# Kernel optimization log

Hardware: AMD Instinct MI355X
Metric: run time of the kernel (lower is better)

Reference implementation:

```python
import jax, jax.numpy as jnp
import numpy as np

N = 50000   # nodes
E = 800000  # edges
C = 64      # node feature channels (0e)
A = 4       # edge attr channels
B = 16      # edge embedding (radial basis) size
H = 8       # radial MLP hidden size
D = 32      # query/key channels
P = 16      # node attr channels
R_MAX = 5.0


def setup_inputs() -> dict:
    key = jax.random.key(0)
    ks = jax.random.split(key, 20)
    w = lambda k, shape, fan_in: (jax.random.normal(k, shape, jnp.float32) / np.sqrt(fan_in).astype(np.float32))
    inp = {
        "node_feats": jax.random.normal(ks[0], (N, C), jnp.float32),
        "node_attrs": jax.random.normal(ks[1], (N, P), jnp.float32),
        "edge_embedding": jax.random.uniform(ks[2], (E, B), jnp.float32),
        "edge_attrs": jax.random.normal(ks[3], (E, A), jnp.float32),
        "positions": jax.random.normal(ks[4], (N, 3), jnp.float32) * 0.3,  # keep lengths < r_max
        "edge_src": jax.random.randint(ks[5], (E,), 0, N),
        "edge_dst": jax.random.randint(ks[6], (E,), 0, N),
        # parameters
        "W_q": w(ks[7], (C, D), C),            # h_q Linear
        "W1_k": w(ks[8], (B, H), B),           # radial MLP for tp_k
        "W2_k": w(ks[9], (H, C * A), H),
        "W1_v": w(ks[10], (B, H), B),          # radial MLP for tp_v
        "W2_v": w(ks[11], (H, C * A), H),
        "W_lin_k": w(ks[12], (C, D), C),       # linear_k
        "W_lin_v": w(ks[13], (C, C), C),       # linear_v
        "W_dot": w(ks[14], (D, D), D * D),     # FullyConnectedTensorProduct(q,k,'0e')
        "W_sc": w(ks[15], (C, P, C), C * P),   # self connection FCTP
    }
    return inp


def soft_unit_step(x):
    safe = jnp.where(x > 0, x, 1.0)
    return jnp.where(x > 0, jnp.exp(-1.0 / safe), 0.0)


def uvu_tp(x_src, edge_attrs, edge_embedding, W1, W2):
    # radial MLP -> per-edge, per-path weights [E, C, A]; 'uvu' tensor product on scalars
    wgt = (jax.nn.silu(edge_embedding @ W1) @ W2).reshape(-1, C, A)
    return x_src * (jnp.einsum('eca,ea->ec', wgt, edge_attrs) / np.sqrt(A).astype(np.float32))


def reference(node_feats, node_attrs, edge_embedding, edge_attrs, positions,
              edge_src, edge_dst, W_q, W1_k, W2_k, W1_v, W2_v,
              W_lin_k, W_lin_v, W_dot, W_sc):
    q = (node_feats @ W_q)[edge_dst]                              # [E, D]
    x_src = node_feats[edge_src]                                  # [E, C]
    k = uvu_tp(x_src, edge_attrs, edge_embedding, W1_k, W2_k) @ W_lin_k  # [E, D]
    v = uvu_tp(x_src, edge_attrs, edge_embedding, W1_v, W2_v) @ W_lin_v  # [E, C]

    edge_vec = positions[edge_dst] - positions[edge_src]
    edge_length = jnp.linalg.norm(edge_vec, axis=1)               # [E]
    cutoff = soft_unit_step(2.0 * R_MAX * (1.0 - edge_length / R_MAX))

    score = jnp.einsum('ei,ij,ej->e', q, W_dot, k)                # weighted bilinear dot -> 0e
    expv = cutoff * jnp.exp(score)                                # [E]
    z = jax.ops.segment_sum(expv, edge_dst, num_segments=N)       # softmax normalizer
    z = jnp.where(z == 0, 1.0, z)
    alpha = expv / z[edge_dst]
    msg = jnp.sqrt(jax.nn.relu(alpha))[:, None] * v               # [E, C]
    node_out = jax.ops.segment_sum(msg, edge_dst, num_segments=N)  # [N, C]

    sc = jnp.einsum('nc,np,cpo->no', node_feats, node_attrs, W_sc)
    return node_out + sc
```

## Files before the change

### kernel.cpp

```cpp
#include <hip/hip_runtime.h>
#include <math.h>

#define NN 50000
#define EE 800000
#define NPAD 50176

typedef __attribute__((ext_vector_type(8))) short short8v;
typedef __attribute__((ext_vector_type(4))) float f32x4;

static __device__ __forceinline__ short bf16r(float x) {
  union { float f; unsigned u; } v; v.f = x;
  unsigned r = v.u + 0x7FFFu + ((v.u >> 16) & 1u);
  return (short)(r >> 16);
}
static __device__ __forceinline__ float bf2f(unsigned u) {
  union { unsigned u; float f; } v; v.u = u << 16;
  return v.f;
}
static __device__ __forceinline__ unsigned pk2(float a, float b) {
  return (unsigned)(unsigned short)bf16r(a) | ((unsigned)(unsigned short)bf16r(b) << 16);
}


__global__ __launch_bounds__(256) void prep_kernel(
    const float* __restrict__ Wq, const float* __restrict__ Wdot,
    const float* __restrict__ Wlk, const float* __restrict__ W2k,
    const float* __restrict__ W2v, const float* __restrict__ Wlv,
    const float* __restrict__ Wsc, float* __restrict__ M,
    unsigned short* __restrict__ w2kT, unsigned short* __restrict__ w2vT,
    unsigned short* __restrict__ wlvb, unsigned short* __restrict__ wscb,
    int* __restrict__ cur)
{
  const int tid = threadIdx.x;
  const int b = blockIdx.x;
  if (b == 0) {
    __shared__ float tmp[2048];
#pragma unroll
    for (int r = 0; r < 8; ++r) {
      int idx = tid + r * 256;
      int cin = idx >> 5, d = idx & 31;
      float a = 0.f;
      for (int j = 0; j < 32; ++j) a = fmaf(Wq[cin * 32 + j], Wdot[j * 32 + d], a);
      tmp[idx] = a;
    }
    __syncthreads();
#pragma unroll
    for (int r = 0; r < 16; ++r) {
      int idx = tid + r * 256;
      int cin = idx >> 6, c = idx & 63;
      float a = 0.f;
      for (int d = 0; d < 32; ++d) a = fmaf(tmp[cin * 32 + d], Wlk[c * 32 + d], a);
      M[idx] = a;
    }
#pragma unroll
    for (int r = 0; r < 8; ++r) {
      int idx = tid + r * 256;
      int c = idx >> 5, k = idx & 31, h = k >> 2, a = k & 3;
      w2kT[idx] = (unsigned short)bf16r(W2k[h * 256 + c * 4 + a]);
      w2vT[idx] = (unsigned short)bf16r(W2v[h * 256 + c * 4 + a]);
    }
#pragma unroll
    for (int r = 0; r < 16; ++r) {
      int idx = tid + r * 256;
      int o = idx >> 6, c = idx & 63;
      wlvb[idx] = (unsigned short)bf16r(Wlv[c * 64 + o]);
    }
  } else if (b <= 196) {
    cur[(b - 1) * 256 + tid] = 0;
  } else {
    int w = (b - 197) * 256 + tid;
    int c = w & 63, o = (w >> 6) & 63, p = w >> 12;
    wscb[w] = (unsigned short)bf16r(Wsc[c * 1024 + p * 64 + o]);
  }
}

__global__ __launch_bounds__(256) void hist_zero(
    const int* __restrict__ edst, int* __restrict__ cur, float4* __restrict__ zu)
{
  int i = blockIdx.x * 256 + threadIdx.x;
  float4 zf = make_float4(0.f, 0.f, 0.f, 0.f);
  zu[i] = zf;
  if (i < 12544) zu[800000 + i] = zf;
  atomicAdd(&cur[edst[i]], 1);
}

__global__ __launch_bounds__(256) void scanA_kernel(
    int* __restrict__ cur, int* __restrict__ bsum)
{
  __shared__ int s[256];
  const int tid = threadIdx.x;
  const int i = blockIdx.x * 256 + tid;
  int v = cur[i];
  s[tid] = v;
  __syncthreads();
  for (int off = 1; off < 256; off <<= 1) {
    int t = (tid >= off) ? s[tid - off] : 0;
    __syncthreads();
    s[tid] += t;
    __syncthreads();
  }
  cur[i] = s[tid] - v;
  if (tid == 255) bsum[blockIdx.x] = s[255];
}

__global__ __launch_bounds__(256) void scanB_kernel(int* __restrict__ bsum)
{
  __shared__ int s[256];
  const int tid = threadIdx.x;
  int v = (tid < 196) ? bsum[tid] : 0;
  s[tid] = v;
  __syncthreads();
  for (int off = 1; off < 256; off <<= 1) {
    int t = (tid >= off) ? s[tid - off] : 0;
    __syncthreads();
    s[tid] += t;
    __syncthreads();
  }
  if (tid < 196) bsum[tid] = s[tid] - v;
}

__global__ __launch_bounds__(256) void scatter_fused(
    const int* __restrict__ esrc, const int* __restrict__ edst,
    const float* __restrict__ ea, const float* __restrict__ eb,
    const float* __restrict__ pos, const float* __restrict__ W1k,
    const float* __restrict__ W1v, int* __restrict__ cur,
    const int* __restrict__ bsum, int* __restrict__ perm,
    float* __restrict__ rec)
{
  int e = blockIdx.x * 256 + threadIdx.x;
  int s = esrc[e], d = edst[e];
  int r = atomicAdd(&cur[d], 1) + bsum[d >> 8];
  perm[r] = e;
  float dx = pos[d * 3 + 0] - pos[s * 3 + 0];
  float dy = pos[d * 3 + 1] - pos[s * 3 + 1];
  float dz = pos[d * 3 + 2] - pos[s * 3 + 2];
  float len = sqrtf(fmaf(dx, dx, fmaf(dy, dy, dz * dz)));
  float arg = 10.f - 2.f * len;
  float cl = (arg > 0.f) ? __expf(-1.f / arg) : 0.f;
  const f32x4* eb4 = reinterpret_cast<const f32x4*>(eb);
  f32x4 q0 = eb4[e * 4 + 0], q1 = eb4[e * 4 + 1],
        q2 = eb4[e * 4 + 2], q3 = eb4[e * 4 + 3];
  float ebv[16] = {q0.x, q0.y, q0.z, q0.w, q1.x, q1.y, q1.z, q1.w,
                   q2.x, q2.y, q2.z, q2.w, q3.x, q3.y, q3.z, q3.w};
  float h[16];
#pragma unroll
  for (int j = 0; j < 16; ++j) h[j] = 0.f;
#pragma unroll
  for (int b = 0; b < 16; ++b) {
    float x = ebv[b];
#pragma unroll
    for (int j = 0; j < 8; ++j) {
      h[j]     = fmaf(x, W1k[b * 8 + j], h[j]);
      h[8 + j] = fmaf(x, W1v[b * 8 + j], h[8 + j]);
    }
  }
#pragma unroll
  for (int j = 0; j < 16; ++j) h[j] = h[j] / (1.f + __expf(-h[j]));

  f32x4 a4 = reinterpret_cast<const f32x4*>(ea)[e];
  f32x4* rp4 = reinterpret_cast<f32x4*>(rec + (size_t)e * 12);
  f32x4 w0, w1, w2;
  w0.x = cl;
  w0.y = __uint_as_float(pk2(a4.x, a4.y));
  w0.z = __uint_as_float(pk2(a4.z, a4.w));
  w0.w = 0.f;
  w1.x = __uint_as_float(pk2(h[0], h[1]));
  w1.y = __uint_as_float(pk2(h[2], h[3]));
  w1.z = __uint_as_float(pk2(h[4], h[5]));
  w1.w = __uint_as_float(pk2(h[6], h[7]));
  w2.x = __uint_as_float(pk2(h[8], h[9]));
  w2.y = __uint_as_float(pk2(h[10], h[11]));
  w2.z = __uint_as_float(pk2(h[12], h[13]));
  w2.w = __uint_as_float(pk2(h[14], h[15]));
  rp4[0] = w0;
  rp4[1] = w1;
  rp4[2] = w2;
}

__global__ __launch_bounds__(256) void tq_kernel(
    const float* __restrict__ nf, const float* __restrict__ M, float* __restrict__ tq)
{
  __shared__ float Ml[4096];
  __shared__ float nfl[64 * 68];
  const int tid = threadIdx.x;
  const int base = blockIdx.x * 64;
#pragma unroll
  for (int r = 0; r < 4; ++r) {
    int idx = tid + r * 256;
    reinterpret_cast<float4*>(Ml)[idx] = reinterpret_cast<const float4*>(M)[idx];
  }
#pragma unroll
  for (int r = 0; r < 4; ++r) {
    int idx = tid + r * 256;
    int row = idx >> 4, c4 = idx & 15;
    float4 v = make_float4(0.f, 0.f, 0.f, 0.f);
    if (base + row < NN) v = reinterpret_cast<const float4*>(nf)[(base + row) * 16 + c4];
    *reinterpret_cast<float4*>(&nfl[row * 68 + c4 * 4]) = v;
  }
  __syncthreads();
  const int to = tid & 15, tn = tid >> 4;
  float4 acc[4] = {make_float4(0,0,0,0), make_float4(0,0,0,0),
                   make_float4(0,0,0,0), make_float4(0,0,0,0)};
  for (int c = 0; c < 64; ++c) {
    float4 m = reinterpret_cast<const float4*>(Ml)[c * 16 + to];
#pragma unroll
    for (int i = 0; i < 4; ++i) {
      float x = nfl[(tn * 4 + i) * 68 + c];
      acc[i].x = fmaf(x, m.x, acc[i].x);
      acc[i].y = fmaf(x, m.y, acc[i].y);
      acc[i].z = fmaf(x, m.z, acc[i].z);
      acc[i].w = fmaf(x, m.w, acc[i].w);
    }
  }
#pragma unroll
  for (int i = 0; i < 4; ++i) {
    int n = base + tn * 4 + i;
    if (n < NN) reinterpret_cast<float4*>(tq)[n * 16 + to] = acc[i];
  }
}

__global__ __launch_bounds__(256) void edge_kernel(
    const float* __restrict__ nf, const float* __restrict__ tq,
    const float* __restrict__ rec, const int* __restrict__ perm,
    const int* __restrict__ esrc, const int* __restrict__ edst,
    const unsigned short* __restrict__ w2kT, const unsigned short* __restrict__ w2vT,
    float* __restrict__ z, float* __restrict__ U)
{
  __shared__ float xsAll[4][16 * 68];
  __shared__ int   esAll[4][16];
  __shared__ int   edAll[4][16];
  __shared__ float clAll[4][16];
  __shared__ float evAll[4][16];
  const int tid  = threadIdx.x;
  const int lane = tid & 63;
  const int w = tid >> 6;
  const int lo = lane & 15, hi = lane >> 4;
  const int sb = (blockIdx.x * 4 + w) * 16;
  float* xs = xsAll[w];
  int*   es = esAll[w];
  int*   ed = edAll[w];
  float* cl = clAll[w];
  float* evs = evAll[w];

  short8v bk[4], bv[4];
#pragma unroll
  for (int t = 0; t < 4; ++t) {
    bk[t] = *reinterpret_cast<const short8v*>(&w2kT[(16 * t + lo) * 32 + hi * 8]);
    bv[t] = *reinterpret_cast<const short8v*>(&w2vT[(16 * t + lo) * 32 + hi * 8]);
  }

  const int eL = perm[sb + lo];
  const unsigned* ru = reinterpret_cast<const unsigned*>(rec);
  const size_t rb = (size_t)eL * 12;
  unsigned ea01 = ru[rb + 1];
  unsigned ea23 = ru[rb + 2];
  unsigned k01  = ru[rb + 4 + hi];
  unsigned v01  = ru[rb + 8 + hi];

  if (hi == 0) {
    es[lo] = esrc[eL];
    ed[lo] = edst[eL];
    cl[lo] = rec[rb];
  }
  __builtin_amdgcn_wave_barrier();

#pragma unroll
  for (int r = 0; r < 4; ++r) {
    int idx = lane + r * 64;
    int e = idx >> 4, c4 = idx & 15;
    float4 xv = reinterpret_cast<const float4*>(nf)[es[e] * 16 + c4];
    *reinterpret_cast<float4*>(&xs[e * 68 + c4 * 4]) = xv;
  }

  float ax = bf2f(ea01 & 0xffffu), ay = bf2f(ea01 >> 16);
  float az = bf2f(ea23 & 0xffffu), aw = bf2f(ea23 >> 16);
  float hk0 = bf2f(k01 & 0xffffu), hk1 = bf2f(k01 >> 16);
  float hv0 = bf2f(v01 & 0xffffu), hv1 = bf2f(v01 >> 16);
  short8v ak, av;
  ak[0] = bf16r(hk0 * ax); ak[1] = bf16r(hk0 * ay);
  ak[2] = bf16r(hk0 * az); ak[3] = bf16r(hk0 * aw);
  ak[4] = bf16r(hk1 * ax); ak[5] = bf16r(hk1 * ay);
  ak[6] = bf16r(hk1 * az); ak[7] = bf16r(hk1 * aw);
  av[0] = bf16r(hv0 * ax); av[1] = bf16r(hv0 * ay);
  av[2] = bf16r(hv0 * az); av[3] = bf16r(hv0 * aw);
  av[4] = bf16r(hv1 * ax); av[5] = bf16r(hv1 * ay);
  av[6] = bf16r(hv1 * az); av[7] = bf16r(hv1 * aw);
  __builtin_amdgcn_wave_barrier();

  f32x4 zero = {0.f, 0.f, 0.f, 0.f};
  f32x4 ack[4], acv[4];
#pragma unroll
  for (int t = 0; t < 4; ++t) {
    ack[t] = __builtin_amdgcn_mfma_f32_16x16x32_bf16(ak, bk[t], zero, 0, 0, 0);
    acv[t] = __builtin_amdgcn_mfma_f32_16x16x32_bf16(av, bv[t], zero, 0, 0, 0);
  }

  const int erow = 4 * hi;
  float p0, p1, p2, p3;
  {
    const float* x0 = &xs[(erow + 0) * 68 + lo];
    const float* x1 = &xs[(erow + 1) * 68 + lo];
    const float* x2 = &xs[(erow + 2) * 68 + lo];
    const float* x3 = &xs[(erow + 3) * 68 + lo];
    const float* t0 = tq + (size_t)ed[erow + 0] * 64 + lo;
    const float* t1 = tq + (size_t)ed[erow + 1] * 64 + lo;
    const float* t2 = tq + (size_t)ed[erow + 2] * 64 + lo;
    const float* t3 = tq + (size_t)ed[erow + 3] * 64 + lo;
    p0 = (x0[0]*t0[0])*ack[0][0] + (x0[16]*t0[16])*ack[1][0] + (x0[32]*t0[32])*ack[2][0] + (x0[48]*t0[48])*ack[3][0];
    p1 = (x1[0]*t1[0])*ack[0][1] + (x1[16]*t1[16])*ack[1][1] + (x1[32]*t1[32])*ack[2][1] + (x1[48]*t1[48])*ack[3][1];
    p2 = (x2[0]*t2[0])*ack[0][2] + (x2[16]*t2[16])*ack[1][2] + (x2[32]*t2[32])*ack[2][2] + (x2[48]*t2[48])*ack[3][2];
    p3 = (x3[0]*t3[0])*ack[0][3] + (x3[16]*t3[16])*ack[1][3] + (x3[32]*t3[32])*ack[2][3] + (x3[48]*t3[48])*ack[3][3];
  }
#pragma unroll
  for (int off = 1; off < 16; off <<= 1) {
    p0 += __shfl_xor(p0, off);
    p1 += __shfl_xor(p1, off);
    p2 += __shfl_xor(p2, off);
    p3 += __shfl_xor(p3, off);
  }
  float ev0 = cl[erow + 0] * __expf(0.5f * p0);
  float ev1 = cl[erow + 1] * __expf(0.5f * p1);
  float ev2 = cl[erow + 2] * __expf(0.5f * p2);
  float ev3 = cl[erow + 3] * __expf(0.5f * p3);
  float se0 = sqrtf(ev0), se1 = sqrtf(ev1), se2 = sqrtf(ev2), se3 = sqrtf(ev3);
  if (lo < 4) {
    float ev = (lo == 0) ? ev0 : (lo == 1) ? ev1 : (lo == 2) ? ev2 : ev3;
    evs[erow + lo] = ev;
  }
#pragma unroll
  for (int i = 0; i < 4; ++i) {
    const float se = (i == 0) ? se0 : (i == 1) ? se1 : (i == 2) ? se2 : se3;
    float* xr = &xs[(erow + i) * 68 + lo];
#pragma unroll
    for (int t = 0; t < 4; ++t) {
      xr[16 * t] = se * xr[16 * t] * acv[t][i];
    }
  }
  __builtin_amdgcn_wave_barrier();
  {
    const int c = lane;
    float acc = 0.f, evacc = 0.f;
    int prev = ed[0];
#pragma unroll
    for (int r = 0; r < 16; ++r) {
      int d = ed[r];
      if (d != prev) {
        unsafeAtomicAdd(&U[prev * 64 + c], acc);
        if (c == 0) unsafeAtomicAdd(&z[prev], evacc);
        acc = 0.f; evacc = 0.f; prev = d;
      }
      acc += xs[r * 68 + c];
      if (c == 0) evacc += evs[r];
    }
    unsafeAtomicAdd(&U[prev * 64 + c], acc);
    if (c == 0) unsafeAtomicAdd(&z[prev], evacc);
  }
}

__global__ __launch_bounds__(256, 4) void final_kernel(
    const float* __restrict__ nf, const float* __restrict__ na,
    const float* __restrict__ U, const float* __restrict__ z,
    const unsigned short* __restrict__ wscb, const unsigned short* __restrict__ wlvb,
    float* __restrict__ out)
{
  __shared__ float nfl[64 * 68];
  __shared__ float Ul[64 * 68];
  __shared__ float nal[64 * 17];
  __shared__ float sl[64];
  const int tid = threadIdx.x;
  const int lane = tid & 63;
  const int lo = lane & 15, hi = lane >> 4;
  const int w = tid >> 6;
  const int nb = blockIdx.x * 64;

#pragma unroll
  for (int r = 0; r < 4; ++r) {
    int idx = tid + r * 256;
    int row = idx >> 4, c4 = idx & 15;
    int n = nb + row; if (n >= NN) n = NN - 1;
    float4 v = reinterpret_cast<const float4*>(nf)[n * 16 + c4];
    *reinterpret_cast<float4*>(&nfl[row * 68 + c4 * 4]) = v;
    float4 u = reinterpret_cast<const float4*>(U)[n * 16 + c4];
    *reinterpret_cast<float4*>(&Ul[row * 68 + c4 * 4]) = u;
  }
#pragma unroll
  for (int r = 0; r < 4; ++r) {
    int idx = tid + r * 256;
    int row = idx >> 4, p = idx & 15;
    int n = nb + row; if (n >= NN) n = NN - 1;
    nal[row * 17 + p] = na[n * 16 + p];
  }
  if (tid < 64) {
    int n = nb + tid; if (n >= NN) n = NN - 1;
    float zz = z[n];
    sl[tid] = (zz > 0.f) ? 0.5f * rsqrtf(zz) : 0.f;
  }
  __syncthreads();

  const int row = 16 * w + lo;
  short8v anf[2], au[2];
#pragma unroll
  for (int kk = 0; kk < 2; ++kk) {
#pragma unroll
    for (int j = 0; j < 8; ++j) {
      anf[kk][j] = bf16r(nfl[row * 68 + 32 * kk + 8 * hi + j]);
      au[kk][j]  = bf16r(Ul[row * 68 + 32 * kk + 8 * hi + j]);
    }
  }

  f32x4 zeroA = {0.f, 0.f, 0.f, 0.f};
  f32x4 accS[4] = {zeroA, zeroA, zeroA, zeroA};
  f32x4 accU[4] = {zeroA, zeroA, zeroA, zeroA};

#pragma unroll
  for (int t = 0; t < 4; ++t) {
    short8v b0 = *reinterpret_cast<const short8v*>(&wlvb[(16 * t + lo) * 64 + 8 * hi]);
    short8v b1 = *reinterpret_cast<const short8v*>(&wlvb[(16 * t + lo) * 64 + 32 + 8 * hi]);
    accU[t] = __builtin_amdgcn_mfma_f32_16x16x32_bf16(au[0], b0, accU[t], 0, 0, 0);
    accU[t] = __builtin_amdgcn_mfma_f32_16x16x32_bf16(au[1], b1, accU[t], 0, 0, 0);
  }
#pragma unroll 1
  for (int p = 0; p < 16; ++p) {
    f32x4 cp[4] = {zeroA, zeroA, zeroA, zeroA};
#pragma unroll
    for (int t = 0; t < 4; ++t) {
      const int bbase = (p * 64 + 16 * t + lo) * 64 + 8 * hi;
      short8v b0 = *reinterpret_cast<const short8v*>(&wscb[bbase]);
      short8v b1 = *reinterpret_cast<const short8v*>(&wscb[bbase + 32]);
      cp[t] = __builtin_amdgcn_mfma_f32_16x16x32_bf16(anf[0], b0, cp[t], 0, 0, 0);
      cp[t] = __builtin_amdgcn_mfma_f32_16x16x32_bf16(anf[1], b1, cp[t], 0, 0, 0);
    }
#pragma unroll
    for (int i = 0; i < 4; ++i) {
      float nav = nal[(16 * w + 4 * hi + i) * 17 + p];
#pragma unroll
      for (int t = 0; t < 4; ++t) accS[t][i] = fmaf(nav, cp[t][i], accS[t][i]);
    }
  }
#pragma unroll
  for (int i = 0; i < 4; ++i) {
    int n = nb + 16 * w + 4 * hi + i;
    if (n < NN) {
      float s = sl[16 * w + 4 * hi + i];
#pragma unroll
      for (int t = 0; t < 4; ++t) {
        out[n * 64 + 16 * t + lo] = fmaf(s, accU[t][i], accS[t][i]);
      }
    }
  }
}

extern "C" void kernel_launch(void* const* d_in, const int* in_sizes, int n_in,
                              void* d_out, int out_size, void* d_ws, size_t ws_size,
                              hipStream_t stream) {
  const float* nf   = (const float*)d_in[0];
  const float* na   = (const float*)d_in[1];
  const float* eb   = (const float*)d_in[2];
  const float* ea   = (const float*)d_in[3];
  const float* pos  = (const float*)d_in[4];
  const int*   esrc = (const int*)d_in[5];
  const int*   edst = (const int*)d_in[6];
  const float* Wq   = (const float*)d_in[7];
  const float* W1k  = (const float*)d_in[8];
  const float* W2k  = (const float*)d_in[9];
  const float* W1v  = (const float*)d_in[10];
  const float* W2v  = (const float*)d_in[11];
  const float* Wlk  = (const float*)d_in[12];
  const float* Wlv  = (const float*)d_in[13];
  const float* Wdot = (const float*)d_in[14];
  const float* Wsc  = (const float*)d_in[15];
  float* out = (float*)d_out;

  float* wsf = (float*)d_ws;
  float* z    = wsf;
  float* U    = wsf + 50176;
  float* tq   = wsf + 3250176;
  unsigned short* w2kT = (unsigned short*)(wsf + 6450176);
  unsigned short* w2vT = (unsigned short*)(wsf + 6451200);
  unsigned short* wlvb = (unsigned short*)(wsf + 6452224);
  unsigned short* wscb = (unsigned short*)(wsf + 6454272);
  int*   cur  = (int*)(wsf + 6487040);
  int*   bsum = (int*)(wsf + 6537216);
  float* M    = wsf + 6537472;
  float* rec  = wsf + 6541568;
  int*   perm = (int*)(wsf + 16141568);

  prep_kernel<<<453, 256, 0, stream>>>(Wq, Wdot, Wlk, W2k, W2v, Wlv, Wsc,
                                       M, w2kT, w2vT, wlvb, wscb, cur);
  tq_kernel<<<(NN + 63) / 64, 256, 0, stream>>>(nf, M, tq);
  hist_zero<<<EE / 256, 256, 0, stream>>>(edst, cur, (float4*)z);
  scanA_kernel<<<NPAD / 256, 256, 0, stream>>>(cur, bsum);
  scanB_kernel<<<1, 256, 0, stream>>>(bsum);
  scatter_fused<<<EE / 256, 256, 0, stream>>>(esrc, edst, ea, eb, pos, W1k, W1v,
                                              cur, bsum, perm, rec);
  edge_kernel<<<EE / 64, 256, 0, stream>>>(nf, tq, rec, perm, esrc, edst,
                                           w2kT, w2vT, z, U);
  final_kernel<<<(NN + 63) / 64, 256, 0, stream>>>(nf, na, U, z, wscb, wlvb, out);
}
```

Before: 303.6 us.

## Store gathered node features and tq in bf16, presort src/dst indices

tq_kernel now writes the per-node query projection and a copy of node features as bf16, and edge_kernel gathers these half-size rows instead of fp32 rows. scatter_fused also writes src and dst indices in sorted order, so edge_kernel reads them contiguously instead of through perm-indexed random loads. The aim is to cut gather bandwidth in the edge kernel. The cost is lower precision in the score's x_src and tq terms and extra writes in the earlier kernels.

```diff
diff --git a/kernel.cpp b/kernel.cpp
--- a/kernel.cpp
+++ b/kernel.cpp
@@ -125,12 +125,15 @@
     const float* __restrict__ pos, const float* __restrict__ W1k,
     const float* __restrict__ W1v, int* __restrict__ cur,
     const int* __restrict__ bsum, int* __restrict__ perm,
+    int* __restrict__ ssrc, int* __restrict__ sdst,
     float* __restrict__ rec)
 {
   int e = blockIdx.x * 256 + threadIdx.x;
   int s = esrc[e], d = edst[e];
   int r = atomicAdd(&cur[d], 1) + bsum[d >> 8];
   perm[r] = e;
+  ssrc[r] = s;
+  sdst[r] = d;
   float dx = pos[d * 3 + 0] - pos[s * 3 + 0];
   float dy = pos[d * 3 + 1] - pos[s * 3 + 1];
   float dz = pos[d * 3 + 2] - pos[s * 3 + 2];
@@ -178,7 +181,8 @@
 }
 
 __global__ __launch_bounds__(256) void tq_kernel(
-    const float* __restrict__ nf, const float* __restrict__ M, float* __restrict__ tq)
+    const float* __restrict__ nf, const float* __restrict__ M,
+    unsigned short* __restrict__ tqb, unsigned short* __restrict__ nfb)
 {
   __shared__ float Ml[4096];
   __shared__ float nfl[64 * 68];
@@ -215,14 +219,28 @@
 #pragma unroll
   for (int i = 0; i < 4; ++i) {
     int n = base + tn * 4 + i;
-    if (n < NN) reinterpret_cast<float4*>(tq)[n * 16 + to] = acc[i];
+    if (n < NN) {
+      unsigned* tp = reinterpret_cast<unsigned*>(tqb) + (size_t)n * 32 + to * 2;
+      tp[0] = pk2(acc[i].x, acc[i].y);
+      tp[1] = pk2(acc[i].z, acc[i].w);
+    }
+  }
+#pragma unroll
+  for (int r = 0; r < 8; ++r) {
+    int idx = tid + r * 256;
+    int row = idx >> 5, cp = idx & 31;
+    int n = base + row;
+    if (n < NN) {
+      reinterpret_cast<unsigned*>(nfb)[(size_t)n * 32 + cp] =
+          pk2(nfl[row * 68 + cp * 2], nfl[row * 68 + cp * 2 + 1]);
+    }
   }
 }
 
 __global__ __launch_bounds__(256) void edge_kernel(
-    const float* __restrict__ nf, const float* __restrict__ tq,
+    const unsigned short* __restrict__ nfb, const unsigned short* __restrict__ tqb,
     const float* __restrict__ rec, const int* __restrict__ perm,
-    const int* __restrict__ esrc, const int* __restrict__ edst,
+    const int* __restrict__ ssrc, const int* __restrict__ sdst,
     const unsigned short* __restrict__ w2kT, const unsigned short* __restrict__ w2vT,
     float* __restrict__ z, float* __restrict__ U)
 {
@@ -256,20 +274,25 @@
   unsigned ea23 = ru[rb + 2];
   unsigned k01  = ru[rb + 4 + hi];
   unsigned v01  = ru[rb + 8 + hi];
-
   if (hi == 0) {
-    es[lo] = esrc[eL];
-    ed[lo] = edst[eL];
+    es[lo] = ssrc[sb + lo];
+    ed[lo] = sdst[sb + lo];
     cl[lo] = rec[rb];
   }
   __builtin_amdgcn_wave_barrier();
 
 #pragma unroll
-  for (int r = 0; r < 4; ++r) {
+  for (int r = 0; r < 2; ++r) {
     int idx = lane + r * 64;
-    int e = idx >> 4, c4 = idx & 15;
-    float4 xv = reinterpret_cast<const float4*>(nf)[es[e] * 16 + c4];
-    *reinterpret_cast<float4*>(&xs[e * 68 + c4 * 4]) = xv;
+    int e = idx >> 3, c8 = idx & 7;
+    float4 pv = reinterpret_cast<const float4*>(nfb)[(size_t)es[e] * 8 + c8];
+    unsigned u0 = __float_as_uint(pv.x), u1 = __float_as_uint(pv.y),
+             u2 = __float_as_uint(pv.z), u3 = __float_as_uint(pv.w);
+    float* xp = &xs[e * 68 + c8 * 8];
+    xp[0] = bf2f(u0 & 0xffffu); xp[1] = bf2f(u0 >> 16);
+    xp[2] = bf2f(u1 & 0xffffu); xp[3] = bf2f(u1 >> 16);
+    xp[4] = bf2f(u2 & 0xffffu); xp[5] = bf2f(u2 >> 16);
+    xp[6] = bf2f(u3 & 0xffffu); xp[7] = bf2f(u3 >> 16);
   }
 
   float ax = bf2f(ea01 & 0xffffu), ay = bf2f(ea01 >> 16);
@@ -296,20 +319,18 @@
   }
 
   const int erow = 4 * hi;
-  float p0, p1, p2, p3;
-  {
-    const float* x0 = &xs[(erow + 0) * 68 + lo];
-    const float* x1 = &xs[(erow + 1) * 68 + lo];
-    const float* x2 = &xs[(erow + 2) * 68 + lo];
-    const float* x3 = &xs[(erow + 3) * 68 + lo];
-    const float* t0 = tq + (size_t)ed[erow + 0] * 64 + lo;
-    const float* t1 = tq + (size_t)ed[erow + 1] * 64 + lo;
-    const float* t2 = tq + (size_t)ed[erow + 2] * 64 + lo;
-    const float* t3 = tq + (size_t)ed[erow + 3] * 64 + lo;
-    p0 = (x0[0]*t0[0])*ack[0][0] + (x0[16]*t0[16])*ack[1][0] + (x0[32]*t0[32])*ack[2][0] + (x0[48]*t0[48])*ack[3][0];
-    p1 = (x1[0]*t1[0])*ack[0][1] + (x1[16]*t1[16])*ack[1][1] + (x1[32]*t1[32])*ack[2][1] + (x1[48]*t1[48])*ack[3][1];
-    p2 = (x2[0]*t2[0])*ack[0][2] + (x2[16]*t2[16])*ack[1][2] + (x2[32]*t2[32])*ack[2][2] + (x2[48]*t2[48])*ack[3][2];
-    p3 = (x3[0]*t3[0])*ack[0][3] + (x3[16]*t3[16])*ack[1][3] + (x3[32]*t3[32])*ack[2][3] + (x3[48]*t3[48])*ack[3][3];
+  const unsigned short* tp0 = tqb + (size_t)ed[erow + 0] * 64;
+  const unsigned short* tp1 = tqb + (size_t)ed[erow + 1] * 64;
+  const unsigned short* tp2 = tqb + (size_t)ed[erow + 2] * 64;
+  const unsigned short* tp3 = tqb + (size_t)ed[erow + 3] * 64;
+  float p0 = 0.f, p1 = 0.f, p2 = 0.f, p3 = 0.f;
+#pragma unroll
+  for (int t = 0; t < 4; ++t) {
+    int c = lo + 16 * t;
+    p0 = fmaf(xs[(erow + 0) * 68 + c] * bf2f(tp0[c]), ack[t][0], p0);
+    p1 = fmaf(xs[(erow + 1) * 68 + c] * bf2f(tp1[c]), ack[t][1], p1);
+    p2 = fmaf(xs[(erow + 2) * 68 + c] * bf2f(tp2[c]), ack[t][2], p2);
+    p3 = fmaf(xs[(erow + 3) * 68 + c] * bf2f(tp3[c]), ack[t][3], p3);
   }
 #pragma unroll
   for (int off = 1; off < 16; off <<= 1) {
@@ -474,7 +495,8 @@
   float* wsf = (float*)d_ws;
   float* z    = wsf;
   float* U    = wsf + 50176;
-  float* tq   = wsf + 3250176;
+  unsigned short* nfb = (unsigned short*)(wsf + 3250176);
+  unsigned short* tqb = (unsigned short*)(wsf + 4850176);
   unsigned short* w2kT = (unsigned short*)(wsf + 6450176);
   unsigned short* w2vT = (unsigned short*)(wsf + 6451200);
   unsigned short* wlvb = (unsigned short*)(wsf + 6452224);
@@ -483,17 +505,19 @@
   int*   bsum = (int*)(wsf + 6537216);
   float* M    = wsf + 6537472;
   float* rec  = wsf + 6541568;
-  int*   perm = (int*)(wsf + 16141568);
+  int*   ssrc = (int*)(wsf + 16141568);
+  int*   sdst = (int*)(wsf + 16941568);
+  int*   perm = (int*)(wsf + 17741568);
 
   prep_kernel<<<453, 256, 0, stream>>>(Wq, Wdot, Wlk, W2k, W2v, Wlv, Wsc,
                                        M, w2kT, w2vT, wlvb, wscb, cur);
-  tq_kernel<<<(NN + 63) / 64, 256, 0, stream>>>(nf, M, tq);
+  tq_kernel<<<(NN + 63) / 64, 256, 0, stream>>>(nf, M, tqb, nfb);
   hist_zero<<<EE / 256, 256, 0, stream>>>(edst, cur, (float4*)z);
   scanA_kernel<<<NPAD / 256, 256, 0, stream>>>(cur, bsum);
   scanB_kernel<<<1, 256, 0, stream>>>(bsum);
   scatter_fused<<<EE / 256, 256, 0, stream>>>(esrc, edst, ea, eb, pos, W1k, W1v,
-                                              cur, bsum, perm, rec);
-  edge_kernel<<<EE / 64, 256, 0, stream>>>(nf, tq, rec, perm, esrc, edst,
+                                              cur, bsum, perm, ssrc, sdst, rec);
+  edge_kernel<<<EE / 64, 256, 0, stream>>>(nfb, tqb, rec, perm, ssrc, sdst,
                                            w2kT, w2vT, z, U);
   final_kernel<<<(NN + 63) / 64, 256, 0, stream>>>(nf, na, U, z, wscb, wlvb, out);
 }
```

After: 316.7 us. 1.04x slower.
